# Kernel tuning notes

Hardware: AMD Instinct MI355X
Metric: run time of the kernel (lower is better)

Reference implementation:

```python
import jax, jax.numpy as jnp
import numpy as np

N = 100000      # nodes
E = 1600000     # edges (avg degree 16)
F_IN = 128      # node feature dim
F_E = 8         # edge feature dim
H = 4           # attention heads (layer 1)
C = 16          # hidden per head
T = 1           # target size (layer 2, heads=1, concat=False)
NEG_SLOPE = 0.2


def setup_inputs() -> dict:
    key = jax.random.key(0)
    ks = jax.random.split(key, 20)
    g = lambda k, shape, fan: (jax.random.normal(k, shape, jnp.float32) / np.sqrt(fan))
    return {
        "x": jax.random.normal(ks[0], (N, F_IN), jnp.float32),
        "edge_index": jax.random.randint(ks[1], (2, E), 0, N, dtype=jnp.int32),
        "edge_attr": jax.random.normal(ks[2], (E, F_E), jnp.float32),
        # layer 1 (in=F_IN, out=C, heads=H, concat=True, edge_dim=F_E)
        "Wl1": g(ks[3], (F_IN, H * C), F_IN),
        "bl1": jnp.zeros((H * C,), jnp.float32),
        "Wr1": g(ks[4], (F_IN, H * C), F_IN),
        "br1": jnp.zeros((H * C,), jnp.float32),
        "We1": g(ks[5], (F_E, H * C), F_E),
        "att1": g(ks[6], (H, C), C),
        "b1": jnp.zeros((H * C,), jnp.float32),
        # layer 2 (in=H*C, out=T, heads=1, concat=False, edge_dim=F_E)
        "Wl2": g(ks[7], (H * C, T), H * C),
        "bl2": jnp.zeros((T,), jnp.float32),
        "Wr2": g(ks[8], (H * C, T), H * C),
        "br2": jnp.zeros((T,), jnp.float32),
        "We2": g(ks[9], (F_E, T), F_E),
        "att2": g(ks[10], (1, T), T),
        "b2": jnp.zeros((T,), jnp.float32),
    }


def _gatv2(x, src, dst, eattr, Wl, bl, Wr, br, We, att, bias, heads, out_ch, concat, n_nodes):
    # add self loops, self-loop edge_attr = mean of edge_attr (PyG fill_value='mean')
    loop = jnp.arange(n_nodes, dtype=src.dtype)
    src_a = jnp.concatenate([src, loop])
    dst_a = jnp.concatenate([dst, loop])
    ea = jnp.concatenate(
        [eattr, jnp.broadcast_to(eattr.mean(axis=0), (n_nodes, eattr.shape[1]))], axis=0)

    xl = (x @ Wl + bl).reshape(n_nodes, heads, out_ch)   # source transform
    xr = (x @ Wr + br).reshape(n_nodes, heads, out_ch)   # target transform
    ee = (ea @ We).reshape(-1, heads, out_ch)            # edge transform (no bias)

    # GATv2: score = att . LeakyReLU(x_l[src] + x_r[dst] + W_e e)
    s = jax.nn.leaky_relu(xl[src_a] + xr[dst_a] + ee, NEG_SLOPE)  # [Ea,H,C]
    logits = jnp.einsum('ehc,hc->eh', s, att)                      # [Ea,H]

    # segment softmax over destination nodes (every node has a self loop)
    m = jax.ops.segment_max(logits, dst_a, num_segments=n_nodes)   # [N,H]
    p = jnp.exp(logits - m[dst_a])
    denom = jax.ops.segment_sum(p, dst_a, num_segments=n_nodes)
    alpha = p / denom[dst_a]                                        # [Ea,H]

    out = jax.ops.segment_sum(xl[src_a] * alpha[:, :, None], dst_a,
                              num_segments=n_nodes)                 # [N,H,C]
    out = out.reshape(n_nodes, heads * out_ch) if concat else out.mean(axis=1)
    return out + bias


def reference(x, edge_index, edge_attr, Wl1, bl1, Wr1, br1, We1, att1, b1,
              Wl2, bl2, Wr2, br2, We2, att2, b2):
    src, dst = edge_index[0], edge_index[1]
    # dropout layers are identity at eval time (training=False)
    h = _gatv2(x, src, dst, edge_attr, Wl1, bl1, Wr1, br1, We1, att1, b1,
               H, C, True, N)
    h = jax.nn.elu(h)
    out = _gatv2(h, src, dst, edge_attr, Wl2, bl2, Wr2, br2, We2, att2, b2,
                 1, T, False, N)
    return out
```

## Files before the change

### kernel.cpp

```cpp
#include <hip/hip_runtime.h>
#include <hip/hip_fp16.h>
#include <math.h>

#define N_NODES 100000
#define N_EDGES 1600000
#define N_ITEMS (N_EDGES + N_NODES)
#define F_IN 128
#define F_E 8
#define HC 64
#define NHEAD 4
#define NEG 0.2f
#define SCAN_BS 1024
#define SCAN_NB ((N_NODES + SCAN_BS - 1) / SCAN_BS)
#define MS_BLOCKS 1024
#define NEG_BIG (-3.0e38f)

union H2I { __half2 h; int i; };

__global__ void mean_sum_kernel(const float* __restrict__ ea, float* __restrict__ partials,
                                unsigned* __restrict__ deg) {
    __shared__ float sh[4][8];
    int stride = gridDim.x * blockDim.x;
    for (int i = blockIdx.x * blockDim.x + threadIdx.x; i < N_NODES; i += stride)
        deg[i] = 1u;
    float acc[8] = {0.f,0.f,0.f,0.f,0.f,0.f,0.f,0.f};
    for (int r = blockIdx.x * blockDim.x + threadIdx.x; r < N_EDGES; r += stride) {
        const float4* p = (const float4*)(ea + (size_t)r * 8);
        float4 a = p[0], b = p[1];
        acc[0] += a.x; acc[1] += a.y; acc[2] += a.z; acc[3] += a.w;
        acc[4] += b.x; acc[5] += b.y; acc[6] += b.z; acc[7] += b.w;
    }
    int wid  = threadIdx.x >> 6;
    int lane = threadIdx.x & 63;
#pragma unroll
    for (int k = 0; k < 8; k++) {
        float v = acc[k];
        for (int off = 32; off; off >>= 1) v += __shfl_down(v, off);
        if (lane == 0) sh[wid][k] = v;
    }
    __syncthreads();
    if (threadIdx.x < 8) {
        float s = sh[0][threadIdx.x] + sh[1][threadIdx.x] + sh[2][threadIdx.x] + sh[3][threadIdx.x];
        partials[blockIdx.x * 8 + threadIdx.x] = s;
    }
}

__global__ void reduce_sum8(const float* __restrict__ partials, float* __restrict__ sum8) {
    int lane = threadIdx.x;
    int c = lane & 7, g = lane >> 3;
    float s = 0.f;
    for (int b = g; b < MS_BLOCKS; b += 8) s += partials[b * 8 + c];
    s += __shfl_xor(s, 8);
    s += __shfl_xor(s, 16);
    s += __shfl_xor(s, 32);
    if (lane < 8) sum8[lane] = s;
}

__global__ void hist_kernel(const int* __restrict__ dst, unsigned* __restrict__ deg) {
    int e = blockIdx.x * blockDim.x + threadIdx.x;
    if (e < N_EDGES) atomicAdd(&deg[dst[e]], 1u);
}

__global__ void scan1(const unsigned* __restrict__ deg, unsigned* __restrict__ local_inc,
                      unsigned* __restrict__ bsum) {
    __shared__ unsigned wsum[16];
    int i = blockIdx.x * SCAN_BS + threadIdx.x;
    int lane = threadIdx.x & 63;
    int wid  = threadIdx.x >> 6;
    unsigned v = (i < N_NODES) ? deg[i] : 0u;
    unsigned sc = v;
#pragma unroll
    for (int off = 1; off < 64; off <<= 1) {
        unsigned t = __shfl_up(sc, off);
        if (lane >= off) sc += t;
    }
    if (lane == 63) wsum[wid] = sc;
    __syncthreads();
    if (threadIdx.x < 16) {
        unsigned w = wsum[threadIdx.x];
#pragma unroll
        for (int off = 1; off < 16; off <<= 1) {
            unsigned t = __shfl_up(w, off);
            if ((int)threadIdx.x >= off) w += t;
        }
        wsum[threadIdx.x] = w;
    }
    __syncthreads();
    unsigned base = wid ? wsum[wid - 1] : 0u;
    sc += base;
    if (i < N_NODES) local_inc[i] = sc;
    if (threadIdx.x == SCAN_BS - 1) bsum[blockIdx.x] = sc;
}

__global__ void scan2(unsigned* __restrict__ bsum) {
    __shared__ unsigned tmp[128];
    int t = threadIdx.x;
    unsigned v = (t < SCAN_NB) ? bsum[t] : 0u;
    tmp[t] = v;
    __syncthreads();
    for (int off = 1; off < 128; off <<= 1) {
        unsigned add = (t >= off) ? tmp[t - off] : 0u;
        __syncthreads();
        tmp[t] += add;
        __syncthreads();
    }
    if (t < SCAN_NB) bsum[t] = tmp[t] - v;
}

__global__ void scan3(const unsigned* __restrict__ local_inc, const unsigned* __restrict__ deg,
                      const unsigned* __restrict__ bsum,
                      unsigned* __restrict__ row_start, unsigned* __restrict__ next) {
    int i = blockIdx.x * blockDim.x + threadIdx.x;
    if (i >= N_NODES) return;
    unsigned v = local_inc[i] - deg[i] + bsum[i / SCAN_BS];
    row_start[i] = v;
    next[i] = v;
}

__global__ void scatter_kernel(const int* __restrict__ src, const int* __restrict__ dst,
                               const float* __restrict__ ea, const float* __restrict__ sum8,
                               const float* __restrict__ We2,
                               unsigned* __restrict__ next,
                               int* __restrict__ sorted_src, __half* __restrict__ seah,
                               float* __restrict__ see2) {
    int item = blockIdx.x * blockDim.x + threadIdx.x;
    if (item >= N_ITEMS) return;
    int s, d;
    float4 a, b;
    if (item < N_EDGES) {
        s = src[item]; d = dst[item];
        const float4* p = (const float4*)(ea + (size_t)item * 8);
        a = p[0]; b = p[1];
    } else {
        s = d = item - N_EDGES;
        const float inv = 1.0f / N_EDGES;
        a = make_float4(sum8[0]*inv, sum8[1]*inv, sum8[2]*inv, sum8[3]*inv);
        b = make_float4(sum8[4]*inv, sum8[5]*inv, sum8[6]*inv, sum8[7]*inv);
    }
    float ee2 = a.x*We2[0] + a.y*We2[1] + a.z*We2[2] + a.w*We2[3]
              + b.x*We2[4] + b.y*We2[5] + b.z*We2[6] + b.w*We2[7];
    unsigned pos = atomicAdd(&next[d], 1u);
    sorted_src[pos] = s;
    see2[pos] = ee2;
    H2I p0, p1, p2, p3;
    p0.h = __floats2half2_rn(a.x, a.y);
    p1.h = __floats2half2_rn(a.z, a.w);
    p2.h = __floats2half2_rn(b.x, b.y);
    p3.h = __floats2half2_rn(b.z, b.w);
    *(int4*)(seah + (size_t)pos * 8) = make_int4(p0.i, p1.i, p2.i, p3.i);
}

__global__ __launch_bounds__(256) void gemm1_kernel(
        const float* __restrict__ x,
        const float* __restrict__ Wl, const float* __restrict__ bl,
        const float* __restrict__ Wr, const float* __restrict__ br,
        __half* __restrict__ xlh, float* __restrict__ xr) {
    __shared__ float xs_t[F_IN][36];
    int t = threadIdx.x & 31;
    int g = threadIdx.x >> 5;
    const float* Wsel = (t < 16) ? Wl : Wr;
    const float* bsel = (t < 16) ? bl : br;
    int jc = (t < 16) ? 4 * t : 4 * t - HC;
    float4 bias = *(const float4*)(bsel + jc);

    int n0 = blockIdx.x * 32;
    int row = threadIdx.x >> 3;
    int cq  = threadIdx.x & 7;
#pragma unroll
    for (int r = 0; r < 4; r++) {
        int c = cq * 4 + r * 32;
        float4 v = *(const float4*)(x + (size_t)(n0 + row) * F_IN + c);
        xs_t[c + 0][row] = v.x;
        xs_t[c + 1][row] = v.y;
        xs_t[c + 2][row] = v.z;
        xs_t[c + 3][row] = v.w;
    }
    __syncthreads();
    int nb = g * 4;
    float4 a0 = bias, a1 = bias, a2 = bias, a3 = bias;
#pragma unroll 4
    for (int k = 0; k < F_IN; k++) {
        float4 w  = *(const float4*)(Wsel + k * HC + jc);
        float4 xv = *(const float4*)&xs_t[k][nb];
        a0.x += w.x * xv.x; a0.y += w.y * xv.x; a0.z += w.z * xv.x; a0.w += w.w * xv.x;
        a1.x += w.x * xv.y; a1.y += w.y * xv.y; a1.z += w.z * xv.y; a1.w += w.w * xv.y;
        a2.x += w.x * xv.z; a2.y += w.y * xv.z; a2.z += w.z * xv.z; a2.w += w.w * xv.z;
        a3.x += w.x * xv.w; a3.y += w.y * xv.w; a3.z += w.z * xv.w; a3.w += w.w * xv.w;
    }
    if (t < 16) {
        float4 arr[4] = {a0, a1, a2, a3};
#pragma unroll
        for (int r = 0; r < 4; r++) {
            H2I u0, u1;
            u0.h = __floats2half2_rn(arr[r].x, arr[r].y);
            u1.h = __floats2half2_rn(arr[r].z, arr[r].w);
            *(int2*)(xlh + (size_t)(n0 + nb + r) * HC + jc) = make_int2(u0.i, u1.i);
        }
    } else {
        *(float4*)(xr + (size_t)(n0 + nb + 0) * HC + jc) = a0;
        *(float4*)(xr + (size_t)(n0 + nb + 1) * HC + jc) = a1;
        *(float4*)(xr + (size_t)(n0 + nb + 2) * HC + jc) = a2;
        *(float4*)(xr + (size_t)(n0 + nb + 3) * HC + jc) = a3;
    }
}

__device__ __forceinline__ float4 sea_lo(const int4& r) {
    H2I h0, h1; h0.i = r.x; h1.i = r.y;
    float2 f0 = __half22float2(h0.h), f1 = __half22float2(h1.h);
    return make_float4(f0.x, f0.y, f1.x, f1.y);
}
__device__ __forceinline__ float4 sea_hi(const int4& r) {
    H2I h2, h3; h2.i = r.z; h3.i = r.w;
    float2 f2 = __half22float2(h2.h), f3 = __half22float2(h3.h);
    return make_float4(f2.x, f2.y, f3.x, f3.y);
}
__device__ __forceinline__ float4 xl_f(const int2& w) {
    H2I u0, u1; u0.i = w.x; u1.i = w.y;
    float2 g0 = __half22float2(u0.h), g1 = __half22float2(u1.h);
    return make_float4(g0.x, g0.y, g1.x, g1.y);
}

__device__ __forceinline__ void edge_update(const float4* __restrict__ we,
                                            const float4& attv, const float4& xrv,
                                            bool valid, const float4& ea0, const float4& ea1,
                                            const float4& xlv,
                                            float& m, float& den, float4& acc) {
    float4 v;
    v.x = xlv.x + xrv.x + ea0.x*we[0].x + ea0.y*we[1].x + ea0.z*we[2].x + ea0.w*we[3].x
                        + ea1.x*we[4].x + ea1.y*we[5].x + ea1.z*we[6].x + ea1.w*we[7].x;
    v.y = xlv.y + xrv.y + ea0.x*we[0].y + ea0.y*we[1].y + ea0.z*we[2].y + ea0.w*we[3].y
                        + ea1.x*we[4].y + ea1.y*we[5].y + ea1.z*we[6].y + ea1.w*we[7].y;
    v.z = xlv.z + xrv.z + ea0.x*we[0].z + ea0.y*we[1].z + ea0.z*we[2].z + ea0.w*we[3].z
                        + ea1.x*we[4].z + ea1.y*we[5].z + ea1.z*we[6].z + ea1.w*we[7].z;
    v.w = xlv.w + xrv.w + ea0.x*we[0].w + ea0.y*we[1].w + ea0.z*we[2].w + ea0.w*we[3].w
                        + ea1.x*we[4].w + ea1.y*we[5].w + ea1.z*we[6].w + ea1.w*we[7].w;
    v.x = fmaxf(v.x, NEG * v.x);
    v.y = fmaxf(v.y, NEG * v.y);
    v.z = fmaxf(v.z, NEG * v.z);
    v.w = fmaxf(v.w, NEG * v.w);
    float prod = v.x*attv.x + v.y*attv.y + v.z*attv.z + v.w*attv.w;
    prod += __shfl_xor(prod, 1);
    prod += __shfl_xor(prod, 2);
    float logit = valid ? prod : NEG_BIG;
    float mnew  = fmaxf(m, logit);
    float scale = __expf(m - mnew);
    float p     = valid ? __expf(logit - mnew) : 0.f;
    den   = den   * scale + p;
    acc.x = acc.x * scale + p * xlv.x;
    acc.y = acc.y * scale + p * xlv.y;
    acc.z = acc.z * scale + p * xlv.z;
    acc.w = acc.w * scale + p * xlv.w;
    m = mnew;
}

#define GAT1_BLOCKS 2048
__global__ __launch_bounds__(256) void gat1_kernel(
                            const unsigned* __restrict__ row_start, const unsigned* __restrict__ deg,
                            const int* __restrict__ ssrc, const __half* __restrict__ seah,
                            const float* __restrict__ We1, const float* __restrict__ att1,
                            const float* __restrict__ b1,
                            const __half* __restrict__ xlh, const float* __restrict__ xr,
                            const float* __restrict__ Wl2, const float* __restrict__ bl2,
                            const float* __restrict__ Wr2, const float* __restrict__ br2,
                            float* __restrict__ xl2, float* __restrict__ xr2) {
    int wave  = blockIdx.x * (blockDim.x >> 6) + (threadIdx.x >> 6);
    int nwave = GAT1_BLOCKS * 4;
    int lane = threadIdx.x & 63;
    int g  = lane >> 4;
    int cl = lane & 15;

    float4 we[8];
#pragma unroll
    for (int k = 0; k < 8; k++) we[k] = *(const float4*)(We1 + k * HC + 4 * cl);
    float4 attv = *(const float4*)(att1 + 4 * cl);
    float4 b1v  = *(const float4*)(b1 + 4 * cl);
    float4 wl2v = *(const float4*)(Wl2 + 4 * cl);
    float4 wr2v = *(const float4*)(Wr2 + 4 * cl);
    float bl2s = bl2[0], br2s = br2[0];

    for (int node = wave; node < N_NODES; node += nwave) {
        unsigned start = row_start[node];
        unsigned cnt   = deg[node];
        unsigned cm1   = cnt - 1;
        float4 xrv = *(const float4*)(xr + (size_t)node * HC + 4 * cl);

        float mA = NEG_BIG, denA = 0.f, mB = NEG_BIG, denB = 0.f;
        float4 accA = make_float4(0.f,0.f,0.f,0.f), accB = make_float4(0.f,0.f,0.f,0.f);

#define IDXA(J) (start + min((J) + (unsigned)g, cm1))
#define IDXB(J) (start + min((J) + 4u + (unsigned)g, cm1))
        int sA = ssrc[IDXA(0u)], sB = ssrc[IDXB(0u)];
        int4 spA = *(const int4*)(seah + (size_t)IDXA(0u) * 8);
        int4 spB = *(const int4*)(seah + (size_t)IDXB(0u) * 8);
        int2 xpA = *(const int2*)(xlh + (size_t)sA * HC + 4 * cl);
        int2 xpB = *(const int2*)(xlh + (size_t)sB * HC + 4 * cl);
        int sA_n = ssrc[IDXA(8u)], sB_n = ssrc[IDXB(8u)];

        for (unsigned j = 0; j < cnt; j += 8) {
            float4 e0A = sea_lo(spA), e1A = sea_hi(spA), xA = xl_f(xpA);
            float4 e0B = sea_lo(spB), e1B = sea_hi(spB), xB = xl_f(xpB);
            bool vA = (j + g) < cnt, vB = (j + 4 + g) < cnt;
            if (j + 8 < cnt) {
                spA = *(const int4*)(seah + (size_t)IDXA(j + 8) * 8);
                spB = *(const int4*)(seah + (size_t)IDXB(j + 8) * 8);
                xpA = *(const int2*)(xlh + (size_t)sA_n * HC + 4 * cl);
                xpB = *(const int2*)(xlh + (size_t)sB_n * HC + 4 * cl);
                if (j + 16 < cnt) {
                    sA_n = ssrc[IDXA(j + 16)];
                    sB_n = ssrc[IDXB(j + 16)];
                }
            }
            edge_update(we, attv, xrv, vA, e0A, e1A, xA, mA, denA, accA);
            edge_update(we, attv, xrv, vB, e0B, e1B, xB, mB, denB, accB);
        }
#undef IDXA
#undef IDXB

        float m = fmaxf(mA, mB);
        float sAc = __expf(mA - m), sBc = __expf(mB - m);
        float den = denA * sAc + denB * sBc;
        float4 acc;
        acc.x = accA.x * sAc + accB.x * sBc;
        acc.y = accA.y * sAc + accB.y * sBc;
        acc.z = accA.z * sAc + accB.z * sBc;
        acc.w = accA.w * sAc + accB.w * sBc;

        float M = m;
        M = fmaxf(M, __shfl_xor(M, 16));
        M = fmaxf(M, __shfl_xor(M, 32));
        float gs = __expf(m - M);
        den *= gs; acc.x *= gs; acc.y *= gs; acc.z *= gs; acc.w *= gs;
        den   += __shfl_xor(den, 16);   den   += __shfl_xor(den, 32);
        acc.x += __shfl_xor(acc.x, 16); acc.x += __shfl_xor(acc.x, 32);
        acc.y += __shfl_xor(acc.y, 16); acc.y += __shfl_xor(acc.y, 32);
        acc.z += __shfl_xor(acc.z, 16); acc.z += __shfl_xor(acc.z, 32);
        acc.w += __shfl_xor(acc.w, 16); acc.w += __shfl_xor(acc.w, 32);

        float inv_den = 1.f / den;
        float4 o;
        o.x = acc.x * inv_den + b1v.x;
        o.y = acc.y * inv_den + b1v.y;
        o.z = acc.z * inv_den + b1v.z;
        o.w = acc.w * inv_den + b1v.w;
        o.x = o.x > 0.f ? o.x : __expf(o.x) - 1.f;
        o.y = o.y > 0.f ? o.y : __expf(o.y) - 1.f;
        o.z = o.z > 0.f ? o.z : __expf(o.z) - 1.f;
        o.w = o.w > 0.f ? o.w : __expf(o.w) - 1.f;
        float sl = o.x*wl2v.x + o.y*wl2v.y + o.z*wl2v.z + o.w*wl2v.w;
        float sr = o.x*wr2v.x + o.y*wr2v.y + o.z*wr2v.z + o.w*wr2v.w;
#pragma unroll
        for (int off = 1; off <= 8; off <<= 1) {
            sl += __shfl_xor(sl, off);
            sr += __shfl_xor(sr, off);
        }
        if (lane == 0) {
            xl2[node] = sl + bl2s;
            xr2[node] = sr + br2s;
        }
    }
}

#define GAT2_BLOCKS 2048
__global__ __launch_bounds__(256) void gat2_kernel(
                            const unsigned* __restrict__ row_start, const unsigned* __restrict__ deg,
                            const int* __restrict__ sorted_src, const float* __restrict__ see2,
                            const float* __restrict__ att2,
                            const float* __restrict__ xl2, const float* __restrict__ xr2,
                            const float* __restrict__ b2, float* __restrict__ out) {
    int wave  = blockIdx.x * (blockDim.x >> 6) + (threadIdx.x >> 6);
    int nwave = GAT2_BLOCKS * 4;
    int lane = threadIdx.x & 63;
    float a2 = att2[0];
    float b2s = b2[0];
    for (int node = wave; node < N_NODES; node += nwave) {
        unsigned start = row_start[node];
        unsigned cnt   = deg[node];
        float xrv = xr2[node];
        float m = -INFINITY, den = 0.f, num = 0.f;
        for (unsigned base = 0; base < cnt; base += 64) {
            unsigned idx = base + lane;
            float logit = -INFINITY, xv = 0.f;
            if (idx < cnt) {
                int s = sorted_src[start + idx];
                float ee = see2[start + idx];
                xv = xl2[s];
                float v = xv + xrv + ee;
                v = fmaxf(v, NEG * v);
                logit = a2 * v;
            }
            float mm = logit;
            for (int off = 1; off < 64; off <<= 1) mm = fmaxf(mm, __shfl_xor(mm, off));
            float mnew = fmaxf(m, mm);
            float p  = (idx < cnt) ? __expf(logit - mnew) : 0.f;
            float pn = p * xv;
            for (int off = 1; off < 64; off <<= 1) {
                p  += __shfl_xor(p, off);
                pn += __shfl_xor(pn, off);
            }
            float scale = __expf(m - mnew);
            den = den * scale + p;
            num = num * scale + pn;
            m = mnew;
        }
        if (lane == 0) out[node] = num / den + b2s;
    }
}

extern "C" void kernel_launch(void* const* d_in, const int* in_sizes, int n_in,
                              void* d_out, int out_size, void* d_ws, size_t ws_size,
                              hipStream_t stream) {
    const float* x    = (const float*)d_in[0];
    const int*   ei   = (const int*)d_in[1];
    const float* ea   = (const float*)d_in[2];
    const float* Wl1  = (const float*)d_in[3];
    const float* bl1  = (const float*)d_in[4];
    const float* Wr1  = (const float*)d_in[5];
    const float* br1  = (const float*)d_in[6];
    const float* We1  = (const float*)d_in[7];
    const float* att1 = (const float*)d_in[8];
    const float* b1   = (const float*)d_in[9];
    const float* Wl2  = (const float*)d_in[10];
    const float* bl2  = (const float*)d_in[11];
    const float* Wr2  = (const float*)d_in[12];
    const float* br2  = (const float*)d_in[13];
    const float* We2  = (const float*)d_in[14];
    const float* att2 = (const float*)d_in[15];
    const float* b2   = (const float*)d_in[16];

    const int* src = ei;
    const int* dst = ei + N_EDGES;

    float* W = (float*)d_ws;
    size_t o = 0;
    float*    sum8      = W + o;               o += 8;
    float*    partials  = W + o;               o += MS_BLOCKS * 8;
    unsigned* deg       = (unsigned*)(W + o);  o += N_NODES;
    unsigned* local_inc = (unsigned*)(W + o);  o += N_NODES;
    unsigned* bsum      = (unsigned*)(W + o);  o += 128;
    unsigned* row_start = (unsigned*)(W + o);  o += N_NODES;
    unsigned* next      = (unsigned*)(W + o);  o += N_NODES;
    int*      ssrc      = (int*)(W + o);       o += N_ITEMS;
    float*    see2      = W + o;               o += N_ITEMS;
    o = (o + 3) & ~(size_t)3;
    __half*   seah      = (__half*)(W + o);    o += (size_t)N_ITEMS * 4;
    __half*   xl1h      = (__half*)(W + o);    o += (size_t)N_NODES * (HC / 2);
    float*    xr1       = W + o;               o += (size_t)N_NODES * HC;
    float*    xl2       = W + o;               o += N_NODES;
    float*    xr2       = W + o;               o += N_NODES;

    mean_sum_kernel<<<MS_BLOCKS, 256, 0, stream>>>(ea, partials, deg);
    reduce_sum8<<<1, 64, 0, stream>>>(partials, sum8);
    hist_kernel<<<(N_EDGES + 255) / 256, 256, 0, stream>>>(dst, deg);
    scan1<<<SCAN_NB, SCAN_BS, 0, stream>>>(deg, local_inc, bsum);
    scan2<<<1, 128, 0, stream>>>(bsum);
    scan3<<<(N_NODES + 255) / 256, 256, 0, stream>>>(local_inc, deg, bsum, row_start, next);
    scatter_kernel<<<(N_ITEMS + 255) / 256, 256, 0, stream>>>(
        src, dst, ea, sum8, We2, next, ssrc, seah, see2);
    gemm1_kernel<<<N_NODES / 32, 256, 0, stream>>>(x, Wl1, bl1, Wr1, br1, xl1h, xr1);
    gat1_kernel<<<GAT1_BLOCKS, 256, 0, stream>>>(
        row_start, deg, ssrc, seah, We1, att1, b1, xl1h, xr1,
        Wl2, bl2, Wr2, br2, xl2, xr2);
    gat2_kernel<<<GAT2_BLOCKS, 256, 0, stream>>>(
        row_start, deg, ssrc, see2, att2, xl2, xr2, b2, (float*)d_out);
}
```

Baseline: 452.3 us.

## Split GAT layer-1 per head with head-major fp16 tables and drop softmax max

Stores xl and xr as head-major fp16 tables and runs layer-1 attention as one wave per (node, head), with a separate epilogue kernel for bias, ELU and the layer-2 projections. Folds the degree histogram into the edge-attr mean kernel and handles the self loop as +1 in the scans. Removes the running-max rescaling from both softmax passes, which saves exp and shuffle work but can overflow if logits grow large. Grid-stride persistent loops are replaced by one-wave-per-node launches.

```diff
diff --git a/kernel.cpp b/kernel.cpp
--- a/kernel.cpp
+++ b/kernel.cpp
@@ -16,19 +16,36 @@
 #define NEG_BIG (-3.0e38f)
 
 union H2I { __half2 h; int i; };
-
-__global__ void mean_sum_kernel(const float* __restrict__ ea, float* __restrict__ partials,
-                                unsigned* __restrict__ deg) {
+typedef int v2i __attribute__((ext_vector_type(2)));
+typedef int v4i __attribute__((ext_vector_type(4)));
+
+__device__ __forceinline__ float4 h4_to_f4(v2i w) {
+    H2I u0, u1; u0.i = w.x; u1.i = w.y;
+    float2 a = __half22float2(u0.h), b = __half22float2(u1.h);
+    return make_float4(a.x, a.y, b.x, b.y);
+}
+__device__ __forceinline__ float4 h8_lo(v4i r) {
+    H2I h0, h1; h0.i = r.x; h1.i = r.y;
+    float2 f0 = __half22float2(h0.h), f1 = __half22float2(h1.h);
+    return make_float4(f0.x, f0.y, f1.x, f1.y);
+}
+__device__ __forceinline__ float4 h8_hi(v4i r) {
+    H2I h2, h3; h2.i = r.z; h3.i = r.w;
+    float2 f2 = __half22float2(h2.h), f3 = __half22float2(h3.h);
+    return make_float4(f2.x, f2.y, f3.x, f3.y);
+}
+
+__global__ void mean_sum_kernel(const float* __restrict__ ea, const int* __restrict__ dst,
+                                float* __restrict__ partials, unsigned* __restrict__ deg) {
     __shared__ float sh[4][8];
     int stride = gridDim.x * blockDim.x;
-    for (int i = blockIdx.x * blockDim.x + threadIdx.x; i < N_NODES; i += stride)
-        deg[i] = 1u;
     float acc[8] = {0.f,0.f,0.f,0.f,0.f,0.f,0.f,0.f};
     for (int r = blockIdx.x * blockDim.x + threadIdx.x; r < N_EDGES; r += stride) {
         const float4* p = (const float4*)(ea + (size_t)r * 8);
         float4 a = p[0], b = p[1];
         acc[0] += a.x; acc[1] += a.y; acc[2] += a.z; acc[3] += a.w;
         acc[4] += b.x; acc[5] += b.y; acc[6] += b.z; acc[7] += b.w;
+        atomicAdd(&deg[dst[r]], 1u);
     }
     int wid  = threadIdx.x >> 6;
     int lane = threadIdx.x & 63;
@@ -56,18 +73,13 @@
     if (lane < 8) sum8[lane] = s;
 }
 
-__global__ void hist_kernel(const int* __restrict__ dst, unsigned* __restrict__ deg) {
-    int e = blockIdx.x * blockDim.x + threadIdx.x;
-    if (e < N_EDGES) atomicAdd(&deg[dst[e]], 1u);
-}
-
 __global__ void scan1(const unsigned* __restrict__ deg, unsigned* __restrict__ local_inc,
                       unsigned* __restrict__ bsum) {
     __shared__ unsigned wsum[16];
     int i = blockIdx.x * SCAN_BS + threadIdx.x;
     int lane = threadIdx.x & 63;
     int wid  = threadIdx.x >> 6;
-    unsigned v = (i < N_NODES) ? deg[i] : 0u;
+    unsigned v = (i < N_NODES) ? (deg[i] + 1u) : 0u;
     unsigned sc = v;
 #pragma unroll
     for (int off = 1; off < 64; off <<= 1) {
@@ -112,7 +124,7 @@
                       unsigned* __restrict__ row_start, unsigned* __restrict__ next) {
     int i = blockIdx.x * blockDim.x + threadIdx.x;
     if (i >= N_NODES) return;
-    unsigned v = local_inc[i] - deg[i] + bsum[i / SCAN_BS];
+    unsigned v = local_inc[i] - (deg[i] + 1u) + bsum[i / SCAN_BS];
     row_start[i] = v;
     next[i] = v;
 }
@@ -154,7 +166,7 @@
         const float* __restrict__ x,
         const float* __restrict__ Wl, const float* __restrict__ bl,
         const float* __restrict__ Wr, const float* __restrict__ br,
-        __half* __restrict__ xlh, float* __restrict__ xr) {
+        __half* __restrict__ xlh, __half* __restrict__ xrh) {
     __shared__ float xs_t[F_IN][36];
     int t = threadIdx.x & 31;
     int g = threadIdx.x >> 5;
@@ -162,6 +174,9 @@
     const float* bsel = (t < 16) ? bl : br;
     int jc = (t < 16) ? 4 * t : 4 * t - HC;
     float4 bias = *(const float4*)(bsel + jc);
+    __half* table = (t < 16) ? xlh : xrh;
+    size_t hbase = (size_t)(jc >> 4) * N_NODES;
+    int hoff = jc & 15;
 
     int n0 = blockIdx.x * 32;
     int row = threadIdx.x >> 3;
@@ -187,223 +202,160 @@
         a2.x += w.x * xv.z; a2.y += w.y * xv.z; a2.z += w.z * xv.z; a2.w += w.w * xv.z;
         a3.x += w.x * xv.w; a3.y += w.y * xv.w; a3.z += w.z * xv.w; a3.w += w.w * xv.w;
     }
-    if (t < 16) {
-        float4 arr[4] = {a0, a1, a2, a3};
-#pragma unroll
-        for (int r = 0; r < 4; r++) {
-            H2I u0, u1;
-            u0.h = __floats2half2_rn(arr[r].x, arr[r].y);
-            u1.h = __floats2half2_rn(arr[r].z, arr[r].w);
-            *(int2*)(xlh + (size_t)(n0 + nb + r) * HC + jc) = make_int2(u0.i, u1.i);
-        }
-    } else {
-        *(float4*)(xr + (size_t)(n0 + nb + 0) * HC + jc) = a0;
-        *(float4*)(xr + (size_t)(n0 + nb + 1) * HC + jc) = a1;
-        *(float4*)(xr + (size_t)(n0 + nb + 2) * HC + jc) = a2;
-        *(float4*)(xr + (size_t)(n0 + nb + 3) * HC + jc) = a3;
-    }
-}
-
-__device__ __forceinline__ float4 sea_lo(const int4& r) {
-    H2I h0, h1; h0.i = r.x; h1.i = r.y;
-    float2 f0 = __half22float2(h0.h), f1 = __half22float2(h1.h);
-    return make_float4(f0.x, f0.y, f1.x, f1.y);
-}
-__device__ __forceinline__ float4 sea_hi(const int4& r) {
-    H2I h2, h3; h2.i = r.z; h3.i = r.w;
-    float2 f2 = __half22float2(h2.h), f3 = __half22float2(h3.h);
-    return make_float4(f2.x, f2.y, f3.x, f3.y);
-}
-__device__ __forceinline__ float4 xl_f(const int2& w) {
-    H2I u0, u1; u0.i = w.x; u1.i = w.y;
-    float2 g0 = __half22float2(u0.h), g1 = __half22float2(u1.h);
-    return make_float4(g0.x, g0.y, g1.x, g1.y);
-}
-
-__device__ __forceinline__ void edge_update(const float4* __restrict__ we,
-                                            const float4& attv, const float4& xrv,
-                                            bool valid, const float4& ea0, const float4& ea1,
-                                            const float4& xlv,
-                                            float& m, float& den, float4& acc) {
-    float4 v;
-    v.x = xlv.x + xrv.x + ea0.x*we[0].x + ea0.y*we[1].x + ea0.z*we[2].x + ea0.w*we[3].x
-                        + ea1.x*we[4].x + ea1.y*we[5].x + ea1.z*we[6].x + ea1.w*we[7].x;
-    v.y = xlv.y + xrv.y + ea0.x*we[0].y + ea0.y*we[1].y + ea0.z*we[2].y + ea0.w*we[3].y
-                        + ea1.x*we[4].y + ea1.y*we[5].y + ea1.z*we[6].y + ea1.w*we[7].y;
-    v.z = xlv.z + xrv.z + ea0.x*we[0].z + ea0.y*we[1].z + ea0.z*we[2].z + ea0.w*we[3].z
-                        + ea1.x*we[4].z + ea1.y*we[5].z + ea1.z*we[6].z + ea1.w*we[7].z;
-    v.w = xlv.w + xrv.w + ea0.x*we[0].w + ea0.y*we[1].w + ea0.z*we[2].w + ea0.w*we[3].w
-                        + ea1.x*we[4].w + ea1.y*we[5].w + ea1.z*we[6].w + ea1.w*we[7].w;
-    v.x = fmaxf(v.x, NEG * v.x);
-    v.y = fmaxf(v.y, NEG * v.y);
-    v.z = fmaxf(v.z, NEG * v.z);
-    v.w = fmaxf(v.w, NEG * v.w);
-    float prod = v.x*attv.x + v.y*attv.y + v.z*attv.z + v.w*attv.w;
-    prod += __shfl_xor(prod, 1);
-    prod += __shfl_xor(prod, 2);
-    float logit = valid ? prod : NEG_BIG;
-    float mnew  = fmaxf(m, logit);
-    float scale = __expf(m - mnew);
-    float p     = valid ? __expf(logit - mnew) : 0.f;
-    den   = den   * scale + p;
-    acc.x = acc.x * scale + p * xlv.x;
-    acc.y = acc.y * scale + p * xlv.y;
-    acc.z = acc.z * scale + p * xlv.z;
-    acc.w = acc.w * scale + p * xlv.w;
-    m = mnew;
-}
-
-#define GAT1_BLOCKS 2048
-__global__ __launch_bounds__(256) void gat1_kernel(
-                            const unsigned* __restrict__ row_start, const unsigned* __restrict__ deg,
-                            const int* __restrict__ ssrc, const __half* __restrict__ seah,
-                            const float* __restrict__ We1, const float* __restrict__ att1,
-                            const float* __restrict__ b1,
-                            const __half* __restrict__ xlh, const float* __restrict__ xr,
-                            const float* __restrict__ Wl2, const float* __restrict__ bl2,
-                            const float* __restrict__ Wr2, const float* __restrict__ br2,
-                            float* __restrict__ xl2, float* __restrict__ xr2) {
-    int wave  = blockIdx.x * (blockDim.x >> 6) + (threadIdx.x >> 6);
-    int nwave = GAT1_BLOCKS * 4;
+    float4 arr[4] = {a0, a1, a2, a3};
+#pragma unroll
+    for (int r = 0; r < 4; r++) {
+        H2I u0, u1;
+        u0.h = __floats2half2_rn(arr[r].x, arr[r].y);
+        u1.h = __floats2half2_rn(arr[r].z, arr[r].w);
+        *(int2*)(table + (hbase + (n0 + nb + r)) * 16 + hoff) = make_int2(u0.i, u1.i);
+    }
+}
+
+__global__ __launch_bounds__(256) void gat1h_kernel(
+        const unsigned* __restrict__ row_start, const unsigned* __restrict__ deg,
+        const int* __restrict__ ssrc, const __half* __restrict__ seah,
+        const float* __restrict__ We1, const float* __restrict__ att1,
+        const __half* __restrict__ xlh, const __half* __restrict__ xrh,
+        __half* __restrict__ out1) {
+    int wave = threadIdx.x >> 6;
+    int node = blockIdx.x * 4 + wave;
+    int h    = blockIdx.y;
+    int lane = threadIdx.x & 63;
+    int e = lane >> 2;
+    int c = lane & 3;
+
+    float4 we[8];
+#pragma unroll
+    for (int k = 0; k < 8; k++) we[k] = *(const float4*)(We1 + k * HC + h * 16 + 4 * c);
+    float4 attv = *(const float4*)(att1 + h * 16 + 4 * c);
+    unsigned start = row_start[node];
+    unsigned cnt   = deg[node] + 1u;
+    unsigned cm1   = cnt - 1u;
+    v2i xrp = __builtin_nontemporal_load((const v2i*)(xrh + ((size_t)h * N_NODES + node) * 16 + 4 * c));
+    float4 xrv = h4_to_f4(xrp);
+
+    float den = 0.f;
+    float4 acc = make_float4(0.f, 0.f, 0.f, 0.f);
+
+    for (unsigned j = 0; j < cnt; j += 16) {
+        unsigned o = j + (unsigned)e;
+        bool valid = o < cnt;
+        unsigned idx = start + (valid ? o : cm1);
+        int s  = __builtin_nontemporal_load(ssrc + idx);
+        v4i sp = __builtin_nontemporal_load((const v4i*)(seah + (size_t)idx * 8));
+        v2i xp = *(const v2i*)(xlh + ((size_t)h * N_NODES + s) * 16 + 4 * c);
+        float4 e0 = h8_lo(sp), e1 = h8_hi(sp);
+        float4 xv = h4_to_f4(xp);
+        float4 v;
+        v.x = xv.x + xrv.x + e0.x*we[0].x + e0.y*we[1].x + e0.z*we[2].x + e0.w*we[3].x
+                           + e1.x*we[4].x + e1.y*we[5].x + e1.z*we[6].x + e1.w*we[7].x;
+        v.y = xv.y + xrv.y + e0.x*we[0].y + e0.y*we[1].y + e0.z*we[2].y + e0.w*we[3].y
+                           + e1.x*we[4].y + e1.y*we[5].y + e1.z*we[6].y + e1.w*we[7].y;
+        v.z = xv.z + xrv.z + e0.x*we[0].z + e0.y*we[1].z + e0.z*we[2].z + e0.w*we[3].z
+                           + e1.x*we[4].z + e1.y*we[5].z + e1.z*we[6].z + e1.w*we[7].z;
+        v.w = xv.w + xrv.w + e0.x*we[0].w + e0.y*we[1].w + e0.z*we[2].w + e0.w*we[3].w
+                           + e1.x*we[4].w + e1.y*we[5].w + e1.z*we[6].w + e1.w*we[7].w;
+        v.x = fmaxf(v.x, NEG * v.x);
+        v.y = fmaxf(v.y, NEG * v.y);
+        v.z = fmaxf(v.z, NEG * v.z);
+        v.w = fmaxf(v.w, NEG * v.w);
+        float prod = v.x*attv.x + v.y*attv.y + v.z*attv.z + v.w*attv.w;
+        prod += __shfl_xor(prod, 1);
+        prod += __shfl_xor(prod, 2);
+        float p = valid ? __expf(prod) : 0.f;
+        den   += p;
+        acc.x += p * xv.x;
+        acc.y += p * xv.y;
+        acc.z += p * xv.z;
+        acc.w += p * xv.w;
+    }
+#pragma unroll
+    for (int off = 4; off <= 32; off <<= 1) {
+        den   += __shfl_xor(den, off);
+        acc.x += __shfl_xor(acc.x, off);
+        acc.y += __shfl_xor(acc.y, off);
+        acc.z += __shfl_xor(acc.z, off);
+        acc.w += __shfl_xor(acc.w, off);
+    }
+    if (e == 0) {
+        float inv = 1.f / den;
+        H2I u0, u1;
+        u0.h = __floats2half2_rn(acc.x * inv, acc.y * inv);
+        u1.h = __floats2half2_rn(acc.z * inv, acc.w * inv);
+        *(int2*)(out1 + ((size_t)h * N_NODES + node) * 16 + 4 * c) = make_int2(u0.i, u1.i);
+    }
+}
+
+__global__ __launch_bounds__(256) void gat1e_kernel(
+        const __half* __restrict__ out1, const float* __restrict__ b1,
+        const float* __restrict__ Wl2, const float* __restrict__ bl2,
+        const float* __restrict__ Wr2, const float* __restrict__ br2,
+        float* __restrict__ xl2, float* __restrict__ xr2) {
+    int wave = threadIdx.x >> 6;
     int lane = threadIdx.x & 63;
     int g  = lane >> 4;
     int cl = lane & 15;
-
-    float4 we[8];
-#pragma unroll
-    for (int k = 0; k < 8; k++) we[k] = *(const float4*)(We1 + k * HC + 4 * cl);
-    float4 attv = *(const float4*)(att1 + 4 * cl);
-    float4 b1v  = *(const float4*)(b1 + 4 * cl);
-    float4 wl2v = *(const float4*)(Wl2 + 4 * cl);
-    float4 wr2v = *(const float4*)(Wr2 + 4 * cl);
-    float bl2s = bl2[0], br2s = br2[0];
-
-    for (int node = wave; node < N_NODES; node += nwave) {
-        unsigned start = row_start[node];
-        unsigned cnt   = deg[node];
-        unsigned cm1   = cnt - 1;
-        float4 xrv = *(const float4*)(xr + (size_t)node * HC + 4 * cl);
-
-        float mA = NEG_BIG, denA = 0.f, mB = NEG_BIG, denB = 0.f;
-        float4 accA = make_float4(0.f,0.f,0.f,0.f), accB = make_float4(0.f,0.f,0.f,0.f);
-
-#define IDXA(J) (start + min((J) + (unsigned)g, cm1))
-#define IDXB(J) (start + min((J) + 4u + (unsigned)g, cm1))
-        int sA = ssrc[IDXA(0u)], sB = ssrc[IDXB(0u)];
-        int4 spA = *(const int4*)(seah + (size_t)IDXA(0u) * 8);
-        int4 spB = *(const int4*)(seah + (size_t)IDXB(0u) * 8);
-        int2 xpA = *(const int2*)(xlh + (size_t)sA * HC + 4 * cl);
-        int2 xpB = *(const int2*)(xlh + (size_t)sB * HC + 4 * cl);
-        int sA_n = ssrc[IDXA(8u)], sB_n = ssrc[IDXB(8u)];
-
-        for (unsigned j = 0; j < cnt; j += 8) {
-            float4 e0A = sea_lo(spA), e1A = sea_hi(spA), xA = xl_f(xpA);
-            float4 e0B = sea_lo(spB), e1B = sea_hi(spB), xB = xl_f(xpB);
-            bool vA = (j + g) < cnt, vB = (j + 4 + g) < cnt;
-            if (j + 8 < cnt) {
-                spA = *(const int4*)(seah + (size_t)IDXA(j + 8) * 8);
-                spB = *(const int4*)(seah + (size_t)IDXB(j + 8) * 8);
-                xpA = *(const int2*)(xlh + (size_t)sA_n * HC + 4 * cl);
-                xpB = *(const int2*)(xlh + (size_t)sB_n * HC + 4 * cl);
-                if (j + 16 < cnt) {
-                    sA_n = ssrc[IDXA(j + 16)];
-                    sB_n = ssrc[IDXB(j + 16)];
-                }
-            }
-            edge_update(we, attv, xrv, vA, e0A, e1A, xA, mA, denA, accA);
-            edge_update(we, attv, xrv, vB, e0B, e1B, xB, mB, denB, accB);
+    int node = (blockIdx.x * 4 + wave) * 4 + g;
+    int h = cl >> 2, q = cl & 3;
+    v2i op = *(const v2i*)(out1 + ((size_t)h * N_NODES + node) * 16 + 4 * q);
+    float4 o = h4_to_f4(op);
+    float4 bv = *(const float4*)(b1 + 4 * cl);
+    o.x += bv.x; o.y += bv.y; o.z += bv.z; o.w += bv.w;
+    o.x = o.x > 0.f ? o.x : __expf(o.x) - 1.f;
+    o.y = o.y > 0.f ? o.y : __expf(o.y) - 1.f;
+    o.z = o.z > 0.f ? o.z : __expf(o.z) - 1.f;
+    o.w = o.w > 0.f ? o.w : __expf(o.w) - 1.f;
+    float4 wl = *(const float4*)(Wl2 + 4 * cl);
+    float4 wr = *(const float4*)(Wr2 + 4 * cl);
+    float sl = o.x*wl.x + o.y*wl.y + o.z*wl.z + o.w*wl.w;
+    float sr = o.x*wr.x + o.y*wr.y + o.z*wr.z + o.w*wr.w;
+#pragma unroll
+    for (int off = 1; off <= 8; off <<= 1) {
+        sl += __shfl_xor(sl, off);
+        sr += __shfl_xor(sr, off);
+    }
+    if (cl == 0) {
+        xl2[node] = sl + bl2[0];
+        xr2[node] = sr + br2[0];
+    }
+}
+
+__global__ __launch_bounds__(256) void gat2_kernel(
+        const unsigned* __restrict__ row_start, const unsigned* __restrict__ deg,
+        const int* __restrict__ sorted_src, const float* __restrict__ see2,
+        const float* __restrict__ att2,
+        const float* __restrict__ xl2, const float* __restrict__ xr2,
+        const float* __restrict__ b2, float* __restrict__ out) {
+    int node = blockIdx.x * (blockDim.x >> 6) + (threadIdx.x >> 6);
+    int lane = threadIdx.x & 63;
+    if (node >= N_NODES) return;
+    unsigned start = row_start[node];
+    unsigned cnt   = deg[node] + 1u;
+    float xrv = xr2[node];
+    float a2  = att2[0];
+    float den = 0.f, num = 0.f;
+    for (unsigned base = 0; base < cnt; base += 64) {
+        unsigned idx = base + lane;
+        float p = 0.f, xv = 0.f;
+        if (idx < cnt) {
+            int s = sorted_src[start + idx];
+            float ee = see2[start + idx];
+            xv = xl2[s];
+            float v = xv + xrv + ee;
+            v = fmaxf(v, NEG * v);
+            p = __expf(a2 * v);
         }
-#undef IDXA
-#undef IDXB
-
-        float m = fmaxf(mA, mB);
-        float sAc = __expf(mA - m), sBc = __expf(mB - m);
-        float den = denA * sAc + denB * sBc;
-        float4 acc;
-        acc.x = accA.x * sAc + accB.x * sBc;
-        acc.y = accA.y * sAc + accB.y * sBc;
-        acc.z = accA.z * sAc + accB.z * sBc;
-        acc.w = accA.w * sAc + accB.w * sBc;
-
-        float M = m;
-        M = fmaxf(M, __shfl_xor(M, 16));
-        M = fmaxf(M, __shfl_xor(M, 32));
-        float gs = __expf(m - M);
-        den *= gs; acc.x *= gs; acc.y *= gs; acc.z *= gs; acc.w *= gs;
-        den   += __shfl_xor(den, 16);   den   += __shfl_xor(den, 32);
-        acc.x += __shfl_xor(acc.x, 16); acc.x += __shfl_xor(acc.x, 32);
-        acc.y += __shfl_xor(acc.y, 16); acc.y += __shfl_xor(acc.y, 32);
-        acc.z += __shfl_xor(acc.z, 16); acc.z += __shfl_xor(acc.z, 32);
-        acc.w += __shfl_xor(acc.w, 16); acc.w += __shfl_xor(acc.w, 32);
-
-        float inv_den = 1.f / den;
-        float4 o;
-        o.x = acc.x * inv_den + b1v.x;
-        o.y = acc.y * inv_den + b1v.y;
-        o.z = acc.z * inv_den + b1v.z;
-        o.w = acc.w * inv_den + b1v.w;
-        o.x = o.x > 0.f ? o.x : __expf(o.x) - 1.f;
-        o.y = o.y > 0.f ? o.y : __expf(o.y) - 1.f;
-        o.z = o.z > 0.f ? o.z : __expf(o.z) - 1.f;
-        o.w = o.w > 0.f ? o.w : __expf(o.w) - 1.f;
-        float sl = o.x*wl2v.x + o.y*wl2v.y + o.z*wl2v.z + o.w*wl2v.w;
-        float sr = o.x*wr2v.x + o.y*wr2v.y + o.z*wr2v.z + o.w*wr2v.w;
-#pragma unroll
-        for (int off = 1; off <= 8; off <<= 1) {
-            sl += __shfl_xor(sl, off);
-            sr += __shfl_xor(sr, off);
+        float pn = p * xv;
+#pragma unroll
+        for (int off = 1; off < 64; off <<= 1) {
+            p  += __shfl_xor(p, off);
+            pn += __shfl_xor(pn, off);
         }
-        if (lane == 0) {
-            xl2[node] = sl + bl2s;
-            xr2[node] = sr + br2s;
-        }
-    }
-}
-
-#define GAT2_BLOCKS 2048
-__global__ __launch_bounds__(256) void gat2_kernel(
-                            const unsigned* __restrict__ row_start, const unsigned* __restrict__ deg,
-                            const int* __restrict__ sorted_src, const float* __restrict__ see2,
-                            const float* __restrict__ att2,
-                            const float* __restrict__ xl2, const float* __restrict__ xr2,
-                            const float* __restrict__ b2, float* __restrict__ out) {
-    int wave  = blockIdx.x * (blockDim.x >> 6) + (threadIdx.x >> 6);
-    int nwave = GAT2_BLOCKS * 4;
-    int lane = threadIdx.x & 63;
-    float a2 = att2[0];
-    float b2s = b2[0];
-    for (int node = wave; node < N_NODES; node += nwave) {
-        unsigned start = row_start[node];
-        unsigned cnt   = deg[node];
-        float xrv = xr2[node];
-        float m = -INFINITY, den = 0.f, num = 0.f;
-        for (unsigned base = 0; base < cnt; base += 64) {
-            unsigned idx = base + lane;
-            float logit = -INFINITY, xv = 0.f;
-            if (idx < cnt) {
-                int s = sorted_src[start + idx];
-                float ee = see2[start + idx];
-                xv = xl2[s];
-                float v = xv + xrv + ee;
-                v = fmaxf(v, NEG * v);
-                logit = a2 * v;
-            }
-            float mm = logit;
-            for (int off = 1; off < 64; off <<= 1) mm = fmaxf(mm, __shfl_xor(mm, off));
-            float mnew = fmaxf(m, mm);
-            float p  = (idx < cnt) ? __expf(logit - mnew) : 0.f;
-            float pn = p * xv;
-            for (int off = 1; off < 64; off <<= 1) {
-                p  += __shfl_xor(p, off);
-                pn += __shfl_xor(pn, off);
-            }
-            float scale = __expf(m - mnew);
-            den = den * scale + p;
-            num = num * scale + pn;
-            m = mnew;
-        }
-        if (lane == 0) out[node] = num / den + b2s;
-    }
+        den += p;
+        num += pn;
+    }
+    if (lane == 0) out[node] = num / den + b2[0];
 }
 
 extern "C" void kernel_launch(void* const* d_in, const int* in_sizes, int n_in,
@@ -443,23 +395,26 @@
     float*    see2      = W + o;               o += N_ITEMS;
     o = (o + 3) & ~(size_t)3;
     __half*   seah      = (__half*)(W + o);    o += (size_t)N_ITEMS * 4;
-    __half*   xl1h      = (__half*)(W + o);    o += (size_t)N_NODES * (HC / 2);
-    float*    xr1       = W + o;               o += (size_t)N_NODES * HC;
+    __half*   xlh       = (__half*)(W + o);    o += (size_t)N_NODES * (HC/2);
+    __half*   xrh       = (__half*)(W + o);    o += (size_t)N_NODES * (HC/2);
+    __half*   out1      = (__half*)(W + o);    o += (size_t)N_NODES * (HC/2);
     float*    xl2       = W + o;               o += N_NODES;
     float*    xr2       = W + o;               o += N_NODES;
 
-    mean_sum_kernel<<<MS_BLOCKS, 256, 0, stream>>>(ea, partials, deg);
+    hipMemsetAsync(deg, 0, (size_t)N_NODES * sizeof(unsigned), stream);
+    mean_sum_kernel<<<MS_BLOCKS, 256, 0, stream>>>(ea, dst, partials, deg);
     reduce_sum8<<<1, 64, 0, stream>>>(partials, sum8);
-    hist_kernel<<<(N_EDGES + 255) / 256, 256, 0, stream>>>(dst, deg);
     scan1<<<SCAN_NB, SCAN_BS, 0, stream>>>(deg, local_inc, bsum);
     scan2<<<1, 128, 0, stream>>>(bsum);
     scan3<<<(N_NODES + 255) / 256, 256, 0, stream>>>(local_inc, deg, bsum, row_start, next);
     scatter_kernel<<<(N_ITEMS + 255) / 256, 256, 0, stream>>>(
         src, dst, ea, sum8, We2, next, ssrc, seah, see2);
-    gemm1_kernel<<<N_NODES / 32, 256, 0, stream>>>(x, Wl1, bl1, Wr1, br1, xl1h, xr1);
-    gat1_kernel<<<GAT1_BLOCKS, 256, 0, stream>>>(
-        row_start, deg, ssrc, seah, We1, att1, b1, xl1h, xr1,
-        Wl2, bl2, Wr2, br2, xl2, xr2);
-    gat2_kernel<<<GAT2_BLOCKS, 256, 0, stream>>>(
+    gemm1_kernel<<<N_NODES / 32, 256, 0, stream>>>(x, Wl1, bl1, Wr1, br1, xlh, xrh);
+    dim3 g1(N_NODES / 4, NHEAD);
+    gat1h_kernel<<<g1, 256, 0, stream>>>(
+        row_start, deg, ssrc, seah, We1, att1, xlh, xrh, out1);
+    gat1e_kernel<<<N_NODES / 16, 256, 0, stream>>>(
+        out1, b1, Wl2, bl2, Wr2, br2, xl2, xr2);
+    gat2_kernel<<<(N_NODES + 3) / 4, 256, 0, stream>>>(
         row_start, deg, ssrc, see2, att2, xl2, xr2, b2, (float*)d_out);
 }
```

Measured after the change: 581.6 us. 1.29x slower.
